# Optimization experiments

Hardware: AMD Instinct MI355X
Metric: run time of the kernel (lower is better)

## Reference

```python
import jax, jax.numpy as jnp
import numpy as np

B, S, D, H = 4, 2048, 1024, 16
HD = D // H  # 64


def setup_inputs() -> dict:
    key = jax.random.key(0)
    k1, k2, k3 = jax.random.split(key, 3)
    return {
        "hidden_states": jax.random.normal(k1, (B, S, D), dtype=jnp.float32),
        "c_attn_w": jax.random.normal(k2, (D, 3 * D), dtype=jnp.float32) * 0.02,
        "c_attn_b": jnp.zeros((3 * D,), dtype=jnp.float32),
        "c_proj_w": jax.random.normal(k3, (D, D), dtype=jnp.float32) * 0.02,
        "c_proj_b": jnp.zeros((D,), dtype=jnp.float32),
    }


def reference(hidden_states, c_attn_w, c_attn_b, c_proj_w, c_proj_b):
    b, s, d = hidden_states.shape
    qkv = hidden_states @ c_attn_w + c_attn_b  # [B,S,3D]
    q, k, v = jnp.split(qkv, 3, axis=-1)
    # split heads -> [B,H,S,hd]
    def heads(x):
        return x.reshape(b, s, H, HD).transpose(0, 2, 1, 3)
    q, k, v = heads(q), heads(k), heads(v)
    scale = 1.0 / jnp.float32(HD) ** 0.5  # scale_attn_weights=True, no layer-idx scaling
    # fp32 scores (module forces float via autocast(False))
    w = jnp.einsum("bhqd,bhkd->bhqk", q.astype(jnp.float32), k.astype(jnp.float32)) * scale
    causal = jnp.tril(jnp.ones((s, s), dtype=bool))  # [S,S]
    mask_value = jnp.finfo(w.dtype).min
    w = jnp.where(causal[None, None], w, mask_value)
    w = jax.nn.softmax(w, axis=-1).astype(v.dtype)
    a = jnp.einsum("bhqk,bhkd->bhqd", w, v)  # [B,H,S,hd]
    a = a.transpose(0, 2, 1, 3).reshape(b, s, d)  # merge heads
    return a @ c_proj_w + c_proj_b
```

## Files before the change

kernel.cpp:

```cpp
#include <hip/hip_runtime.h>
#include <stdint.h>

typedef __bf16 bf16x8 __attribute__((ext_vector_type(8)));
typedef short s16x8 __attribute__((ext_vector_type(8)));
typedef float f32x4 __attribute__((ext_vector_type(4)));

__device__ __forceinline__ short f2bf(float f) {
  union { __bf16 h; short s; } u;
  u.h = (__bf16)f;
  return u.s;
}

__device__ __forceinline__ void async_copy16(short* lds, const short* g) {
  __builtin_amdgcn_global_load_lds((const __attribute__((address_space(1))) void*)g,
                                   (__attribute__((address_space(3))) void*)lds,
                                   16, 0, 0);
}

__global__ __launch_bounds__(256) void cast_bf16_kernel(const float* __restrict__ in,
                                                        short* __restrict__ out) {
  int i = blockIdx.x * 256 + threadIdx.x;
  float4 v = reinterpret_cast<const float4*>(in)[i];
  short4 o;
  o.x = f2bf(v.x); o.y = f2bf(v.y); o.z = f2bf(v.z); o.w = f2bf(v.w);
  reinterpret_cast<short4*>(out)[i] = o;
}

__global__ __launch_bounds__(256) void transpose_cast_kernel(const float* __restrict__ in,
                                                             short* __restrict__ out,
                                                             int R, int C) {
  __shared__ float tile[32][33];
  int c0 = blockIdx.x * 32, r0 = blockIdx.y * 32;
  int tc = threadIdx.x & 31, tr = threadIdx.x >> 5;
#pragma unroll
  for (int p = 0; p < 4; ++p)
    tile[tr + p * 8][tc] = in[(size_t)(r0 + tr + p * 8) * C + c0 + tc];
  __syncthreads();
#pragma unroll
  for (int p = 0; p < 4; ++p)
    out[(size_t)(c0 + tr + p * 8) * R + r0 + tc] = f2bf(tile[tc][tr + p * 8]);
}

template <bool OBF, bool QSCALE>
__global__ __launch_bounds__(256) void gemm128_kernel(const short* __restrict__ A,
                                                      const short* __restrict__ Bt,
                                                      const float* __restrict__ bias,
                                                      void* __restrict__ Cout,
                                                      int K, int ldc) {
  __shared__ short Asm[128 * 32];
  __shared__ short Bsm[128 * 32];
  const int tid = threadIdx.x;
  const int lane = tid & 63, wid = tid >> 6;
  const int m0 = blockIdx.y * 128, n0 = blockIdx.x * 128;
  const int wm = wid >> 1, wn = wid & 1;
  const int lr = lane & 15, lg = lane >> 4;

  f32x4 acc[4][4] = {};

  const int s1 = tid, s2 = 256 + tid;
  const short* a1 = A + (size_t)(m0 + (s1 >> 2)) * K + (s1 & 3) * 8;
  const short* a2 = A + (size_t)(m0 + (s2 >> 2)) * K + (s2 & 3) * 8;
  const short* b1 = Bt + (size_t)(n0 + (s1 >> 2)) * K + (s1 & 3) * 8;
  const short* b2 = Bt + (size_t)(n0 + (s2 >> 2)) * K + (s2 & 3) * 8;

  for (int k0 = 0; k0 < K; k0 += 32) {
    __syncthreads();
    async_copy16(&Asm[s1 * 8], a1 + k0);
    async_copy16(&Asm[s2 * 8], a2 + k0);
    async_copy16(&Bsm[s1 * 8], b1 + k0);
    async_copy16(&Bsm[s2 * 8], b2 + k0);
    __syncthreads();

    bf16x8 af[4], bf[4];
#pragma unroll
    for (int mi = 0; mi < 4; ++mi)
      af[mi] = *(const bf16x8*)&Asm[(wm * 64 + mi * 16 + lr) * 32 + lg * 8];
#pragma unroll
    for (int ni = 0; ni < 4; ++ni)
      bf[ni] = *(const bf16x8*)&Bsm[(wn * 64 + ni * 16 + lr) * 32 + lg * 8];
    __builtin_amdgcn_s_setprio(1);
#pragma unroll
    for (int mi = 0; mi < 4; ++mi)
#pragma unroll
      for (int ni = 0; ni < 4; ++ni)
        acc[mi][ni] = __builtin_amdgcn_mfma_f32_16x16x32_bf16(af[mi], bf[ni], acc[mi][ni], 0, 0, 0);
    __builtin_amdgcn_s_setprio(0);
  }

#pragma unroll
  for (int ni = 0; ni < 4; ++ni) {
    const int col = n0 + wn * 64 + ni * 16 + lr;
    const float bv = bias[col];
    const float scale = (QSCALE && col < 1024) ? 0.18033688f : 1.0f;
#pragma unroll
    for (int mi = 0; mi < 4; ++mi) {
      const int row = m0 + wm * 64 + mi * 16 + lg * 4;
#pragma unroll
      for (int j = 0; j < 4; ++j) {
        const float v = (acc[mi][ni][j] + bv) * scale;
        if constexpr (OBF)
          ((short*)Cout)[(size_t)(row + j) * ldc + col] = f2bf(v);
        else
          ((float*)Cout)[(size_t)(row + j) * ldc + col] = v;
      }
    }
  }
}

__global__ __launch_bounds__(256) void vtrans_kernel(const short* __restrict__ qkv,
                                                     short* __restrict__ vt) {
  __shared__ short tile[64][72];
  const int tid = threadIdx.x;
  const int s0 = blockIdx.x * 64;
  const int h = blockIdx.y, b = blockIdx.z;
  const short* src = qkv + (size_t)(b * 2048 + s0) * 3072 + 2048 + h * 64;
#pragma unroll
  for (int p = 0; p < 2; ++p) {
    const int r = (tid >> 3) + p * 32;
    const int c0 = (tid & 7) * 8;
    *(s16x8*)&tile[r][c0] = *(const s16x8*)(src + (size_t)r * 3072 + c0);
  }
  __syncthreads();
  short* dst = vt + (size_t)(b * 16 + h) * 64 * 2048;
#pragma unroll
  for (int p = 0; p < 2; ++p) {
    const int d = (tid >> 3) + p * 32;
    const int sl0 = (tid & 7) * 8;
    s16x8 v;
#pragma unroll
    for (int i = 0; i < 8; ++i) v[i] = tile[sl0 + i][d];
    *(s16x8*)(dst + (size_t)d * 2048 + s0 + sl0) = v;
  }
}

__global__ __launch_bounds__(256) void attn_kernel(const short* __restrict__ qkv,
                                                   const short* __restrict__ vt,
                                                   short* __restrict__ abuf) {
  __shared__ short P_lds[4][64][72];
  const int tid = threadIdx.x;
  const int lane = tid & 63, wid = tid >> 6;
  const int lr = lane & 15, lg = lane >> 4;

  const int g = blockIdx.x;
  const int w = ((g & 7) << 5) | (g >> 3);
  const int px = w & 3, h = (w >> 2) & 15, b = w >> 6;

  const int ldq = 3072;
  const short* Qb = qkv + (size_t)b * 2048 * ldq + h * 64;
  const short* Kb = Qb + 1024;
  const short* Vtb = vt + (size_t)(b * 16 + h) * 64 * 2048;

  for (int pp = 0; pp < 2; ++pp) {
    const int qtile = pp ? px : 7 - px;
    const int wrow = pp ? (3 - wid) : wid;
    const int qrowW = qtile * 256 + wrow * 64;

    bf16x8 qf[4][2];
#pragma unroll
    for (int qb = 0; qb < 4; ++qb)
#pragma unroll
      for (int gg = 0; gg < 2; ++gg)
        qf[qb][gg] = *(const bf16x8*)(Qb + (size_t)(qrowW + qb * 16 + lr) * ldq + gg * 32 + lg * 8);

    f32x4 o[4][4] = {};
    float mst[4][4], lsum[4][4];
#pragma unroll
    for (int qb = 0; qb < 4; ++qb)
#pragma unroll
      for (int j = 0; j < 4; ++j) { mst[qb][j] = -__builtin_inff(); lsum[qb][j] = 0.f; }

    const int ntiles = (qrowW >> 6) + 1;

    bf16x8 kf[4][2];
#pragma unroll
    for (int ni = 0; ni < 4; ++ni)
#pragma unroll
      for (int gg = 0; gg < 2; ++gg)
        kf[ni][gg] = *(const bf16x8*)(Kb + (size_t)(ni * 16 + lr) * ldq + gg * 32 + lg * 8);

    for (int t = 0; t < ntiles; ++t) {
      const int kvt = t << 6;
      const bool diag = (t == ntiles - 1);

      bf16x8 vb[4][2];
#pragma unroll
      for (int db = 0; db < 4; ++db)
#pragma unroll
        for (int gg = 0; gg < 2; ++gg)
          vb[db][gg] = *(const bf16x8*)(Vtb + (size_t)(db * 16 + lr) * 2048 + kvt + gg * 32 + lg * 8);

#pragma unroll
      for (int qb = 0; qb < 4; ++qb) {
        f32x4 s[4];
        __builtin_amdgcn_s_setprio(1);
#pragma unroll
        for (int ni = 0; ni < 4; ++ni) {
          f32x4 z = {0.f, 0.f, 0.f, 0.f};
          s[ni] = z;
#pragma unroll
          for (int gg = 0; gg < 2; ++gg)
            s[ni] = __builtin_amdgcn_mfma_f32_16x16x32_bf16(qf[qb][gg], kf[ni][gg], s[ni], 0, 0, 0);
        }
        __builtin_amdgcn_s_setprio(0);

        if (diag) {
#pragma unroll
          for (int ni = 0; ni < 4; ++ni)
#pragma unroll
            for (int j = 0; j < 4; ++j) {
              const int q = qrowW + qb * 16 + lg * 4 + j;
              const int kv = kvt + ni * 16 + lr;
              if (kv > q) s[ni][j] = -__builtin_inff();
            }
        }

        float v4[4];
#pragma unroll
        for (int j = 0; j < 4; ++j) {
          float v = fmaxf(fmaxf(s[0][j], s[1][j]), fmaxf(s[2][j], s[3][j]));
          v = fmaxf(v, __shfl_xor(v, 1, 64));
          v = fmaxf(v, __shfl_xor(v, 2, 64));
          v = fmaxf(v, __shfl_xor(v, 4, 64));
          v = fmaxf(v, __shfl_xor(v, 8, 64));
          v4[j] = v;
        }
        const float gmax = fmaxf(fmaxf(v4[0] - mst[qb][0], v4[1] - mst[qb][1]),
                                 fmaxf(v4[2] - mst[qb][2], v4[3] - mst[qb][3]));
        if (!__all(gmax <= 8.f)) {
#pragma unroll
          for (int j = 0; j < 4; ++j) {
            const float mn = fmaxf(mst[qb][j], v4[j]);
            const float alpha = exp2f(mst[qb][j] - mn);
            mst[qb][j] = mn;
            lsum[qb][j] *= alpha;
#pragma unroll
            for (int db = 0; db < 4; ++db)
              o[qb][db][j] *= alpha;
          }
        }

#pragma unroll
        for (int ni = 0; ni < 4; ++ni)
#pragma unroll
          for (int j = 0; j < 4; ++j) {
            const float p = exp2f(s[ni][j] - mst[qb][j]);
            lsum[qb][j] += p;
            P_lds[wid][qb * 16 + lg * 4 + j][ni * 16 + lr] = f2bf(p);
          }
      }

      if (t + 1 < ntiles) {
        const int kvn = kvt + 64;
#pragma unroll
        for (int ni = 0; ni < 4; ++ni)
#pragma unroll
          for (int gg = 0; gg < 2; ++gg)
            kf[ni][gg] = *(const bf16x8*)(Kb + (size_t)(kvn + ni * 16 + lr) * ldq + gg * 32 + lg * 8);
      }

      bf16x8 pa[4][2];
#pragma unroll
      for (int qb = 0; qb < 4; ++qb)
#pragma unroll
        for (int gg = 0; gg < 2; ++gg)
          pa[qb][gg] = *(const bf16x8*)&P_lds[wid][qb * 16 + lr][gg * 32 + lg * 8];

      __builtin_amdgcn_s_setprio(1);
#pragma unroll
      for (int qb = 0; qb < 4; ++qb)
#pragma unroll
        for (int db = 0; db < 4; ++db)
#pragma unroll
          for (int gg = 0; gg < 2; ++gg)
            o[qb][db] = __builtin_amdgcn_mfma_f32_16x16x32_bf16(pa[qb][gg], vb[db][gg], o[qb][db], 0, 0, 0);
      __builtin_amdgcn_s_setprio(0);
    }

#pragma unroll
    for (int qb = 0; qb < 4; ++qb) {
      float rl[4];
#pragma unroll
      for (int j = 0; j < 4; ++j) {
        float v = lsum[qb][j];
        v += __shfl_xor(v, 1, 64);
        v += __shfl_xor(v, 2, 64);
        v += __shfl_xor(v, 4, 64);
        v += __shfl_xor(v, 8, 64);
        rl[j] = 1.0f / v;
      }
#pragma unroll
      for (int db = 0; db < 4; ++db) {
        const int col = h * 64 + db * 16 + lr;
#pragma unroll
        for (int j = 0; j < 4; ++j) {
          const int row = b * 2048 + qrowW + qb * 16 + lg * 4 + j;
          abuf[(size_t)row * 1024 + col] = f2bf(o[qb][db][j] * rl[j]);
        }
      }
    }
  }
}

extern "C" void kernel_launch(void* const* d_in, const int* in_sizes, int n_in,
                              void* d_out, int out_size, void* d_ws, size_t ws_size,
                              hipStream_t stream) {
  (void)in_sizes; (void)n_in; (void)out_size; (void)ws_size;
  const float* hs = (const float*)d_in[0];
  const float* w1 = (const float*)d_in[1];
  const float* b1 = (const float*)d_in[2];
  const float* w2 = (const float*)d_in[3];
  const float* b2 = (const float*)d_in[4];

  char* w = (char*)d_ws;
  short* Xb  = (short*)(w);
  short* W1T = (short*)(w + 16777216);
  short* W2T = (short*)(w + 23068672);
  short* QKV = (short*)(w + 25165824);
  short* VT  = (short*)(w + 75497472);
  short* AB  = (short*)(w + 92274688);

  cast_bf16_kernel<<<8192, 256, 0, stream>>>(hs, Xb);
  transpose_cast_kernel<<<dim3(96, 32), 256, 0, stream>>>(w1, W1T, 1024, 3072);
  transpose_cast_kernel<<<dim3(32, 32), 256, 0, stream>>>(w2, W2T, 1024, 1024);
  gemm128_kernel<true, true><<<dim3(24, 64), 256, 0, stream>>>(Xb, W1T, b1, QKV, 1024, 3072);
  vtrans_kernel<<<dim3(32, 16, 4), 256, 0, stream>>>(QKV, VT);
  attn_kernel<<<256, 256, 0, stream>>>(QKV, VT, AB);
  gemm128_kernel<false, false><<<dim3(8, 64), 256, 0, stream>>>(AB, W2T, b2, d_out, 1024, 1024);
}
```

Measured before the change: 359.1 us.

## Rewrite GEMM as 256x256 tile with triple-buffered async LDS pipeline

Replaces the 128x128 single-buffered GEMM with a 256x256-tile, 512-thread kernel that prefetches two K-steps ahead into three LDS buffers, using explicit vmcnt waits so loads overlap with MFMA work. It also XOR-swizzles the LDS layout to reduce bank conflicts and remaps block IDs across XCDs for better L2 locality. Each wave now holds 8x4 accumulator tiles, which raises register pressure. The larger tiles mean fewer workgroups: 384 for the QKV GEMM and only 128 for the output projection, which may underfill the 256 CUs.

```diff
diff --git a/kernel.cpp b/kernel.cpp
--- a/kernel.cpp
+++ b/kernel.cpp
@@ -42,50 +42,88 @@
 }
 
 template <bool OBF, bool QSCALE>
-__global__ __launch_bounds__(256) void gemm128_kernel(const short* __restrict__ A,
+__global__ __launch_bounds__(512) void gemm256_kernel(const short* __restrict__ A,
                                                       const short* __restrict__ Bt,
                                                       const float* __restrict__ bias,
                                                       void* __restrict__ Cout,
-                                                      int K, int ldc) {
-  __shared__ short Asm[128 * 32];
-  __shared__ short Bsm[128 * 32];
+                                                      int K, int ldc, int nbx) {
+  __shared__ short lds[3 * 16384];
   const int tid = threadIdx.x;
   const int lane = tid & 63, wid = tid >> 6;
-  const int m0 = blockIdx.y * 128, n0 = blockIdx.x * 128;
-  const int wm = wid >> 1, wn = wid & 1;
+  const int wm = wid >> 2, wn = wid & 3;
   const int lr = lane & 15, lg = lane >> 4;
 
-  f32x4 acc[4][4] = {};
-
-  const int s1 = tid, s2 = 256 + tid;
-  const short* a1 = A + (size_t)(m0 + (s1 >> 2)) * K + (s1 & 3) * 8;
-  const short* a2 = A + (size_t)(m0 + (s2 >> 2)) * K + (s2 & 3) * 8;
-  const short* b1 = Bt + (size_t)(n0 + (s1 >> 2)) * K + (s1 & 3) * 8;
-  const short* b2 = Bt + (size_t)(n0 + (s2 >> 2)) * K + (s2 & 3) * 8;
-
-  for (int k0 = 0; k0 < K; k0 += 32) {
-    __syncthreads();
-    async_copy16(&Asm[s1 * 8], a1 + k0);
-    async_copy16(&Asm[s2 * 8], a2 + k0);
-    async_copy16(&Bsm[s1 * 8], b1 + k0);
-    async_copy16(&Bsm[s2 * 8], b2 + k0);
-    __syncthreads();
-
-    bf16x8 af[4], bf[4];
-#pragma unroll
-    for (int mi = 0; mi < 4; ++mi)
-      af[mi] = *(const bf16x8*)&Asm[(wm * 64 + mi * 16 + lr) * 32 + lg * 8];
+  const int nwg = gridDim.x;
+  const int cpx = nwg >> 3;
+  const int gid = (blockIdx.x & 7) * cpx + (blockIdx.x >> 3);
+  const int m0 = (gid / nbx) * 256, n0 = (gid % nbx) * 256;
+
+  const int srow = tid >> 2;
+  const int scol8 = (tid & 3) ^ ((tid >> 3) & 3);
+  const short* pA0 = A + (size_t)(m0 + srow) * K + scol8 * 8;
+  const short* pA1 = A + (size_t)(m0 + 128 + srow) * K + scol8 * 8;
+  const short* pB0 = Bt + (size_t)(n0 + srow) * K + scol8 * 8;
+  const short* pB1 = Bt + (size_t)(n0 + 128 + srow) * K + scol8 * 8;
+  const int dst = tid * 8;
+
+#define STAGE(tk, buf) do {                                          \
+    const int _o = (buf) * 16384;                                    \
+    async_copy16(&lds[_o + dst],          pA0 + (tk) * 32);          \
+    async_copy16(&lds[_o + 4096 + dst],   pA1 + (tk) * 32);          \
+    async_copy16(&lds[_o + 8192 + dst],   pB0 + (tk) * 32);          \
+    async_copy16(&lds[_o + 12288 + dst],  pB1 + (tk) * 32);          \
+  } while (0)
+
+  const int swz = (lr >> 1) & 3;
+  const int acol = (lg ^ swz) << 3;
+  const int aoff = (wm * 128 + lr) * 32 + acol;
+  const int boff = 8192 + (wn * 64 + lr) * 32 + acol;
+
+  f32x4 acc[8][4] = {};
+  const int nk = K >> 5;
+
+  STAGE(0, 0);
+  STAGE(1, 1);
+
+  int bc = 0, bs = 2;
+  for (int t = 0; t < nk; ++t) {
+    if (t + 2 < nk) {
+      STAGE(t + 2, bs);
+      asm volatile("s_waitcnt vmcnt(8)" ::: "memory");
+    } else if (t + 1 < nk) {
+      asm volatile("s_waitcnt vmcnt(4)" ::: "memory");
+    } else {
+      asm volatile("s_waitcnt vmcnt(0)" ::: "memory");
+    }
+    __builtin_amdgcn_sched_barrier(0);
+    __builtin_amdgcn_s_barrier();
+    __builtin_amdgcn_sched_barrier(0);
+
+    const short* lb = &lds[bc * 16384];
+    bf16x8 af[8], bf[4];
+#pragma unroll
+    for (int mi = 0; mi < 8; ++mi)
+      af[mi] = *(const bf16x8*)(lb + aoff + mi * 512);
 #pragma unroll
     for (int ni = 0; ni < 4; ++ni)
-      bf[ni] = *(const bf16x8*)&Bsm[(wn * 64 + ni * 16 + lr) * 32 + lg * 8];
+      bf[ni] = *(const bf16x8*)(lb + boff + ni * 512);
+
     __builtin_amdgcn_s_setprio(1);
 #pragma unroll
-    for (int mi = 0; mi < 4; ++mi)
+    for (int mi = 0; mi < 8; ++mi)
 #pragma unroll
       for (int ni = 0; ni < 4; ++ni)
         acc[mi][ni] = __builtin_amdgcn_mfma_f32_16x16x32_bf16(af[mi], bf[ni], acc[mi][ni], 0, 0, 0);
     __builtin_amdgcn_s_setprio(0);
-  }
+
+    __builtin_amdgcn_sched_barrier(0);
+    __builtin_amdgcn_s_barrier();
+    __builtin_amdgcn_sched_barrier(0);
+
+    bc = (bc == 2) ? 0 : bc + 1;
+    bs = (bs == 2) ? 0 : bs + 1;
+  }
+#undef STAGE
 
 #pragma unroll
   for (int ni = 0; ni < 4; ++ni) {
@@ -93,8 +131,8 @@
     const float bv = bias[col];
     const float scale = (QSCALE && col < 1024) ? 0.18033688f : 1.0f;
 #pragma unroll
-    for (int mi = 0; mi < 4; ++mi) {
-      const int row = m0 + wm * 64 + mi * 16 + lg * 4;
+    for (int mi = 0; mi < 8; ++mi) {
+      const int row = m0 + wm * 128 + mi * 16 + lg * 4;
 #pragma unroll
       for (int j = 0; j < 4; ++j) {
         const float v = (acc[mi][ni][j] + bv) * scale;
@@ -322,8 +360,8 @@
   cast_bf16_kernel<<<8192, 256, 0, stream>>>(hs, Xb);
   transpose_cast_kernel<<<dim3(96, 32), 256, 0, stream>>>(w1, W1T, 1024, 3072);
   transpose_cast_kernel<<<dim3(32, 32), 256, 0, stream>>>(w2, W2T, 1024, 1024);
-  gemm128_kernel<true, true><<<dim3(24, 64), 256, 0, stream>>>(Xb, W1T, b1, QKV, 1024, 3072);
+  gemm256_kernel<true, true><<<384, 512, 0, stream>>>(Xb, W1T, b1, QKV, 1024, 3072, 12);
   vtrans_kernel<<<dim3(32, 16, 4), 256, 0, stream>>>(QKV, VT);
   attn_kernel<<<256, 256, 0, stream>>>(QKV, VT, AB);
-  gemm128_kernel<false, false><<<dim3(8, 64), 256, 0, stream>>>(AB, W2T, b2, d_out, 1024, 1024);
-}
+  gemm256_kernel<false, false><<<128, 512, 0, stream>>>(AB, W2T, b2, d_out, 1024, 1024, 4);
+}
```

Result: no change. 366.0 us (+1.9%).
